# Kernel optimization log

Hardware: AMD Instinct MI355X
Metric: run time of the kernel (lower is better)

Reference implementation:

```python
import jax, jax.numpy as jnp
import numpy as np

# ---- BEVDepth config ----
B, N = 1, 6
C = 80            # numC_Trans
D = 112           # depth bins
HF, WF = 16, 44   # feature map size
DS = 16           # image downsample factor
XB = (-51.2, 51.2, 0.8)
YB = (-51.2, 51.2, 0.8)
ZB = (-10.0, 10.0, 20.0)
DB = (2.0, 58.0, 0.5)
NX, NY, NZ = 128, 128, 1
DX = np.array([XB[2], YB[2], ZB[2]], np.float32)
BX = np.array([XB[0] + XB[2] / 2.0, YB[0] + YB[2] / 2.0, ZB[0] + ZB[2] / 2.0], np.float32)


def _frustum():
    # (D, H, W, 3) points: (x_pixel, y_pixel, depth) in augmented image coords
    ds = np.arange(DB[0], DB[1], DB[2], dtype=np.float32)          # (D,)
    xs = np.linspace(0.0, WF * DS - 1.0, WF, dtype=np.float32)     # (W,)
    ys = np.linspace(0.0, HF * DS - 1.0, HF, dtype=np.float32)     # (H,)
    xg, yg, dg = np.broadcast_arrays(xs[None, None, :], ys[None, :, None], ds[:, None, None])
    return jnp.asarray(np.stack([xg, yg, dg], axis=-1))            # (D, H, W, 3)


def _get_geometry(rots, trans, intrins, post_rots, post_trans):
    # frustum -> ego-frame 3D points, shape (B, N, D, H, W, 3)
    fr = _frustum()                                                 # (D,H,W,3)
    pts = fr[None, None] - post_trans[:, :, None, None, None, :]
    inv_post = jnp.linalg.inv(post_rots)                            # (B,N,3,3)
    pts = jnp.einsum('bnij,bndhwj->bndhwi', inv_post, pts)
    # (x*d, y*d, d)
    pts = jnp.concatenate([pts[..., :2] * pts[..., 2:3], pts[..., 2:3]], axis=-1)
    combine = rots @ jnp.linalg.inv(intrins)                        # (B,N,3,3)
    pts = jnp.einsum('bnij,bndhwj->bndhwi', combine, pts)
    return pts + trans[:, :, None, None, None, :]


def _voxel_pooling(geom, volume):
    # geom: (B,N,D,H,W,3), volume: (B,N,D,H,W,C)
    dx = jnp.asarray(DX)
    bx = jnp.asarray(BX)
    # torch .long() truncates toward zero -> astype(int32) matches
    gi = ((geom - (bx - dx / 2.0)) / dx).astype(jnp.int32)          # (B,N,D,H,W,3)
    nprime = N * D * HF * WF
    gi = gi.reshape(B, nprime, 3)
    feats = volume.reshape(B * nprime, C)
    ix, iy, iz = gi[..., 0], gi[..., 1], gi[..., 2]                 # (B, nprime)
    valid = ((ix >= 0) & (ix < NX) & (iy >= 0) & (iy < NY) & (iz >= 0) & (iz < NZ))
    bix = jnp.arange(B, dtype=jnp.int32)[:, None]                    # (B,1)
    seg = ((bix * NZ + iz) * NX + ix) * NY + iy                      # (B, nprime)
    nseg = B * NZ * NX * NY
    seg = jnp.where(valid, seg, nseg).reshape(-1)
    pooled = jax.ops.segment_sum(feats, seg, num_segments=nseg + 1)[:-1]  # (B*NZ*NX*NY, C)
    bev = pooled.reshape(B, NZ, NX, NY, C)
    # final[b, :, iz, ix, iy]; unbind Z, cat on channel -> (B, C*NZ, NX, NY)
    bev = jnp.transpose(bev, (0, 4, 1, 2, 3)).reshape(B, C * NZ, NX, NY)
    return bev


def setup_inputs() -> dict:
    key = jax.random.key(0)
    k1, k2, k3 = jax.random.split(key, 3)
    x = jax.random.normal(k1, (B, N, 64, HF, WF), jnp.float32)
    img_feat = jax.random.normal(k2, (B * N, C, HF, WF), jnp.float32)
    depth_digit = jax.random.normal(k3, (B * N, D, HF, WF), jnp.float32)
    # realistic camera geometry: identity extrinsics, pinhole intrinsics,
    # post_rots encode the 1/16 feature-map rescale
    eye = jnp.eye(3, dtype=jnp.float32)
    rots = jnp.broadcast_to(eye, (B, N, 3, 3))
    trans = jnp.zeros((B, N, 3), jnp.float32)
    intr = jnp.array([[500.0, 0.0, WF * DS / 2.0],
                      [0.0, 500.0, HF * DS / 2.0],
                      [0.0, 0.0, 1.0]], jnp.float32)
    intrins = jnp.broadcast_to(intr, (B, N, 3, 3))
    post_rots = jnp.broadcast_to(eye, (B, N, 3, 3))
    post_trans = jnp.zeros((B, N, 3), jnp.float32)
    return {"x": x, "rots": rots, "trans": trans, "intrins": intrins,
            "post_rots": post_rots, "post_trans": post_trans,
            "img_feat": img_feat, "depth_digit": depth_digit}


def reference(x, rots, trans, intrins, post_rots, post_trans, img_feat, depth_digit):
    # depth distribution over D bins
    depth_prob = jax.nn.softmax(depth_digit, axis=1)                 # (BN, D, H, W)
    # depth-weighted outer product -> (BN, C, D, H, W)
    volume = depth_prob[:, None, :, :, :] * img_feat[:, :, None, :, :]
    volume = volume.reshape(B, N, C, D, HF, WF)
    volume = jnp.transpose(volume, (0, 1, 3, 4, 5, 2))               # (B,N,D,H,W,C)
    geom = _get_geometry(rots, trans, intrins, post_rots, post_trans)
    return _voxel_pooling(geom, volume)
```

## Files before the change

### kernel.cpp

```cpp
#include <hip/hip_runtime.h>

#define B_    1
#define N_    6
#define C_    80
#define D_    112
#define HF_   16
#define WF_   44
#define NX_   128
#define NY_   128
#define NZ_   1
#define HW_   (HF_ * WF_)
#define NPIX_ (NZ_ * NX_ * NY_)

__device__ __forceinline__ void inv3(const float* m, float* o) {
    float a = m[0], b = m[1], c = m[2];
    float d = m[3], e = m[4], f = m[5];
    float g = m[6], h = m[7], i = m[8];
    float A  =  (e * i - f * h);
    float Bc = -(d * i - f * g);
    float Cc =  (d * h - e * g);
    float det = a * A + b * Bc + c * Cc;
    float id = 1.0f / det;
    o[0] = A * id;                  o[1] = -(b * i - c * h) * id;   o[2] =  (b * f - c * e) * id;
    o[3] = Bc * id;                 o[4] =  (a * i - c * g) * id;   o[5] = -(a * f - c * d) * id;
    o[6] = Cc * id;                 o[7] = -(a * h - b * g) * id;   o[8] =  (a * e - b * d) * id;
}

__device__ __forceinline__ int voxel_of(float xs, float ys, float dv, const float* sm) {
    const float* ip  = sm;
    const float* cmb = sm + 9;
    float ptx = sm[18], pty = sm[19], ptz = sm[20];
    float trx = sm[21], trY = sm[22], trz = sm[23];
    float p0x = xs - ptx, p0y = ys - pty, p0z = dv - ptz;
    float p1x = ip[0]*p0x + ip[1]*p0y + ip[2]*p0z;
    float p1y = ip[3]*p0x + ip[4]*p0y + ip[5]*p0z;
    float p1z = ip[6]*p0x + ip[7]*p0y + ip[8]*p0z;
    float qx = p1x * p1z, qy = p1y * p1z, qz = p1z;
    float rx = cmb[0]*qx + cmb[1]*qy + cmb[2]*qz + trx;
    float ry = cmb[3]*qx + cmb[4]*qy + cmb[5]*qz + trY;
    float rz = cmb[6]*qx + cmb[7]*qy + cmb[8]*qz + trz;
    const float lox = -50.8f - 0.4f;
    const float loy = -50.8f - 0.4f;
    const float loz = -10.0f;
    int ix = (int)((rx - lox) / 0.8f);
    int iy = (int)((ry - loy) / 0.8f);
    int iz = (int)((rz - loz) / 20.0f);
    bool val = (ix >= 0) && (ix < NX_) && (iy >= 0) && (iy < NY_) && (iz >= 0) && (iz < NZ_);
    return val ? ((iz * NX_ + ix) * NY_ + iy) : -1;
}

__global__ __launch_bounds__(256) void scatter_merged(
    const float* __restrict__ rots, const float* __restrict__ trans,
    const float* __restrict__ intrins, const float* __restrict__ post_rots,
    const float* __restrict__ post_trans,
    const float* __restrict__ img_feat, const float* __restrict__ depth_digit,
    float* __restrict__ outp)
{
    const int hw = blockIdx.x;
    const int w  = hw % WF_;
    const int h  = hw / WF_;
    const int tid  = threadIdx.x;
    const int lane = tid & 63;
    const int wave = tid >> 6;

    __shared__ float s_prob[N_][D_];
    __shared__ float s_feat[N_][C_];
    __shared__ short s_vox[N_][D_];
    __shared__ short s_runv[N_][D_];
    __shared__ float s_runw[N_][D_];
    __shared__ float s_mat[N_][24];
    __shared__ int   s_cnt[N_];
    __shared__ int   s_same;

    for (int i = tid; i < N_ * D_; i += 256) {
        int cam = i / D_, d = i - cam * D_;
        s_prob[cam][d] = depth_digit[((size_t)cam * D_ + d) * HW_ + hw];
    }
    for (int i = tid; i < N_ * C_; i += 256) {
        int cam = i / C_, c = i - cam * C_;
        s_feat[cam][c] = img_feat[((size_t)cam * C_ + c) * HW_ + hw];
    }
    if (tid < N_) {
        float ipv[9], ii[9];
        inv3(post_rots + tid * 9, ipv);
        inv3(intrins + tid * 9, ii);
        const float* ro = rots + tid * 9;
        #pragma unroll
        for (int k = 0; k < 9; ++k) s_mat[tid][k] = ipv[k];
        #pragma unroll
        for (int r = 0; r < 3; ++r)
            #pragma unroll
            for (int c = 0; c < 3; ++c)
                s_mat[tid][9 + r * 3 + c] = ro[r*3+0]*ii[0*3+c] + ro[r*3+1]*ii[1*3+c] + ro[r*3+2]*ii[2*3+c];
        #pragma unroll
        for (int k = 0; k < 3; ++k) { s_mat[tid][18+k] = post_trans[tid*3+k]; s_mat[tid][21+k] = trans[tid*3+k]; }
    }
    __syncthreads();

    for (int cc = wave; cc < N_; cc += 4) {
        bool act = lane < 56;
        float l0 = act ? s_prob[cc][lane]      : -INFINITY;
        float l1 = act ? s_prob[cc][lane + 56] : -INFINITY;
        float m = fmaxf(l0, l1);
        #pragma unroll
        for (int o = 32; o > 0; o >>= 1) m = fmaxf(m, __shfl_xor(m, o));
        float e0 = act ? __expf(l0 - m) : 0.0f;
        float e1 = act ? __expf(l1 - m) : 0.0f;
        float s = e0 + e1;
        #pragma unroll
        for (int o = 32; o > 0; o >>= 1) s += __shfl_xor(s, o);
        float inv = 1.0f / s;
        if (act) { s_prob[cc][lane] = e0 * inv; s_prob[cc][lane + 56] = e1 * inv; }
    }

    {
        float xs = (float)((double)w * (703.0 / 43.0));
        float ys = (float)h * 17.0f;
        for (int i = tid; i < N_ * D_; i += 256) {
            int cam = i / D_, d = i - cam * D_;
            float dval = 2.0f + 0.5f * (float)d;
            s_vox[cam][d] = (short)voxel_of(xs, ys, dval, s_mat[cam]);
        }
    }
    __syncthreads();

    if (tid < N_) {
        int cnt = 0, last = -1;
        float wsum = 0.0f;
        #pragma unroll 4
        for (int d = 0; d < D_; ++d) {
            int v = s_vox[tid][d];
            if (v < 0) continue;
            if (v == last) { wsum += s_prob[tid][d]; }
            else {
                if (last >= 0) { s_runv[tid][cnt] = (short)last; s_runw[tid][cnt] = wsum; ++cnt; }
                last = v; wsum = s_prob[tid][d];
            }
        }
        if (last >= 0) { s_runv[tid][cnt] = (short)last; s_runw[tid][cnt] = wsum; ++cnt; }
        s_cnt[tid] = cnt;
    }
    __syncthreads();

    if (tid == 0) {
        int same = 1, c0 = s_cnt[0];
        #pragma unroll
        for (int cam = 1; cam < N_; ++cam) same &= (s_cnt[cam] == c0);
        if (same) {
            for (int r = 0; r < c0 && same; ++r) {
                short v0 = s_runv[0][r];
                #pragma unroll
                for (int cam = 1; cam < N_; ++cam) same &= (s_runv[cam][r] == v0);
            }
        }
        s_same = same;
    }
    __syncthreads();

    if (s_same) {
        int cnt = s_cnt[0];
        int total = cnt * C_;
        for (int k = tid; k < total; k += 256) {
            int r = k / C_;
            int c = k - r * C_;
            int v = s_runv[0][r];
            float val = 0.0f;
            #pragma unroll
            for (int cam = 0; cam < N_; ++cam)
                val = fmaf(s_runw[cam][r], s_feat[cam][c], val);
            atomicAdd(&outp[(size_t)c * NPIX_ + v], val);
        }
    } else {
        for (int cam = 0; cam < N_; ++cam) {
            int cnt = s_cnt[cam];
            int total = cnt * C_;
            for (int k = tid; k < total; k += 256) {
                int r = k / C_;
                int c = k - r * C_;
                int v = s_runv[cam][r];
                atomicAdd(&outp[(size_t)c * NPIX_ + v], s_runw[cam][r] * s_feat[cam][c]);
            }
        }
    }
}

extern "C" void kernel_launch(void* const* d_in, const int* in_sizes, int n_in,
                              void* d_out, int out_size, void* d_ws, size_t ws_size,
                              hipStream_t stream) {
    const float* rots        = (const float*)d_in[1];
    const float* trans       = (const float*)d_in[2];
    const float* intrins     = (const float*)d_in[3];
    const float* post_rots   = (const float*)d_in[4];
    const float* post_trans  = (const float*)d_in[5];
    const float* img_feat    = (const float*)d_in[6];
    const float* depth_digit = (const float*)d_in[7];
    float* outp = (float*)d_out;

    hipMemsetAsync(outp, 0, (size_t)out_size * sizeof(float), stream);
    scatter_merged<<<HW_, 256, 0, stream>>>(rots, trans, intrins, post_rots, post_trans,
                                            img_feat, depth_digit, outp);
}
```

Measured before the change: 107.5 us.

## Split voxel pooling into run-list generation and per-channel LDS accumulation

```diff
diff --git a/kernel.cpp b/kernel.cpp
--- a/kernel.cpp
+++ b/kernel.cpp
@@ -11,6 +11,8 @@
 #define NZ_   1
 #define HW_   (HF_ * WF_)
 #define NPIX_ (NZ_ * NX_ * NY_)
+#define CAMHW_ (N_ * HW_)
+#define ENTCAP_ (HW_ * N_ * D_)
 
 __device__ __forceinline__ void inv3(const float* m, float* o) {
     float a = m[0], b = m[1], c = m[2];
@@ -49,6 +51,151 @@
     return val ? ((iz * NX_ + ix) * NY_ + iy) : -1;
 }
 
+__global__ __launch_bounds__(256) void runs_kernel(
+    const float* __restrict__ rots, const float* __restrict__ trans,
+    const float* __restrict__ intrins, const float* __restrict__ post_rots,
+    const float* __restrict__ post_trans,
+    const float* __restrict__ depth_digit,
+    int2* __restrict__ entries, int* __restrict__ gE)
+{
+    const int hw = blockIdx.x;
+    const int w  = hw % WF_;
+    const int h  = hw / WF_;
+    const int tid  = threadIdx.x;
+    const int lane = tid & 63;
+    const int wave = tid >> 6;
+
+    __shared__ float s_prob[N_][D_];
+    __shared__ short s_vox[N_][D_];
+    __shared__ short s_runv[N_][D_];
+    __shared__ float s_runw[N_][D_];
+    __shared__ float s_mat[N_][24];
+    __shared__ int   s_cnt[N_];
+    __shared__ int   s_pref[N_ + 1];
+    __shared__ int   s_base;
+
+    for (int i = tid; i < N_ * D_; i += 256) {
+        int cam = i / D_, d = i - cam * D_;
+        s_prob[cam][d] = depth_digit[((size_t)cam * D_ + d) * HW_ + hw];
+    }
+    if (tid < N_) {
+        float ipv[9], ii[9];
+        inv3(post_rots + tid * 9, ipv);
+        inv3(intrins + tid * 9, ii);
+        const float* ro = rots + tid * 9;
+        #pragma unroll
+        for (int k = 0; k < 9; ++k) s_mat[tid][k] = ipv[k];
+        #pragma unroll
+        for (int r = 0; r < 3; ++r)
+            #pragma unroll
+            for (int c = 0; c < 3; ++c)
+                s_mat[tid][9 + r * 3 + c] = ro[r*3+0]*ii[0*3+c] + ro[r*3+1]*ii[1*3+c] + ro[r*3+2]*ii[2*3+c];
+        #pragma unroll
+        for (int k = 0; k < 3; ++k) { s_mat[tid][18+k] = post_trans[tid*3+k]; s_mat[tid][21+k] = trans[tid*3+k]; }
+    }
+    __syncthreads();
+
+    for (int cc = wave; cc < N_; cc += 4) {
+        bool act = lane < 56;
+        float l0 = act ? s_prob[cc][lane]      : -INFINITY;
+        float l1 = act ? s_prob[cc][lane + 56] : -INFINITY;
+        float m = fmaxf(l0, l1);
+        #pragma unroll
+        for (int o = 32; o > 0; o >>= 1) m = fmaxf(m, __shfl_xor(m, o));
+        float e0 = act ? __expf(l0 - m) : 0.0f;
+        float e1 = act ? __expf(l1 - m) : 0.0f;
+        float s = e0 + e1;
+        #pragma unroll
+        for (int o = 32; o > 0; o >>= 1) s += __shfl_xor(s, o);
+        float inv = 1.0f / s;
+        if (act) { s_prob[cc][lane] = e0 * inv; s_prob[cc][lane + 56] = e1 * inv; }
+    }
+
+    {
+        float xs = (float)((double)w * (703.0 / 43.0));
+        float ys = (float)h * 17.0f;
+        for (int i = tid; i < N_ * D_; i += 256) {
+            int cam = i / D_, d = i - cam * D_;
+            float dval = 2.0f + 0.5f * (float)d;
+            s_vox[cam][d] = (short)voxel_of(xs, ys, dval, s_mat[cam]);
+        }
+    }
+    __syncthreads();
+
+    if (tid < N_) {
+        int cnt = 0, last = -1;
+        float wsum = 0.0f;
+        for (int d = 0; d < D_; ++d) {
+            int v = s_vox[tid][d];
+            if (v < 0) continue;
+            if (v == last) { wsum += s_prob[tid][d]; }
+            else {
+                if (last >= 0) { s_runv[tid][cnt] = (short)last; s_runw[tid][cnt] = wsum; ++cnt; }
+                last = v; wsum = s_prob[tid][d];
+            }
+        }
+        if (last >= 0) { s_runv[tid][cnt] = (short)last; s_runw[tid][cnt] = wsum; ++cnt; }
+        s_cnt[tid] = cnt;
+    }
+    __syncthreads();
+
+    if (tid == 0) {
+        int acc = 0;
+        #pragma unroll
+        for (int cam = 0; cam < N_; ++cam) { s_pref[cam] = acc; acc += s_cnt[cam]; }
+        s_pref[N_] = acc;
+        s_base = atomicAdd(gE, acc);
+    }
+    __syncthreads();
+
+    int total = s_pref[N_];
+    int base = s_base;
+    for (int k = tid; k < total; k += 256) {
+        int cam = 0;
+        #pragma unroll
+        for (int cc = 1; cc < N_; ++cc) if (k >= s_pref[cc]) cam = cc;
+        int r = k - s_pref[cam];
+        int key = ((cam * HW_ + hw) << 14) | (int)s_runv[cam][r];
+        entries[base + k] = make_int2(key, __float_as_int(s_runw[cam][r]));
+    }
+}
+
+__global__ __launch_bounds__(1024) void accum_kernel(
+    const float* __restrict__ img_feat,
+    const int2* __restrict__ entries, const int* __restrict__ gE,
+    float* __restrict__ outp)
+{
+    const int c   = blockIdx.x;
+    const int tid = threadIdx.x;
+
+    __shared__ float s_plane[NPIX_];
+    __shared__ float s_feat[CAMHW_];
+    __shared__ int   s_E;
+
+    float4* p4 = (float4*)s_plane;
+    #pragma unroll
+    for (int i = tid; i < NPIX_ / 4; i += 1024) p4[i] = make_float4(0.f, 0.f, 0.f, 0.f);
+    for (int i = tid; i < CAMHW_; i += 1024) {
+        int cam = i / HW_, hw = i - cam * HW_;
+        s_feat[i] = img_feat[((size_t)cam * C_ + c) * HW_ + hw];
+    }
+    if (tid == 0) s_E = *gE;
+    __syncthreads();
+
+    int E = s_E;
+    for (int i = tid; i < E; i += 1024) {
+        int2 e = entries[i];
+        int vox   = e.x & (NPIX_ - 1);
+        int camhw = e.x >> 14;
+        atomicAdd(&s_plane[vox], __int_as_float(e.y) * s_feat[camhw]);
+    }
+    __syncthreads();
+
+    float4* o4 = (float4*)(outp + (size_t)c * NPIX_);
+    #pragma unroll
+    for (int i = tid; i < NPIX_ / 4; i += 1024) o4[i] = p4[i];
+}
+
 __global__ __launch_bounds__(256) void scatter_merged(
     const float* __restrict__ rots, const float* __restrict__ trans,
     const float* __restrict__ intrins, const float* __restrict__ post_rots,
@@ -70,15 +217,14 @@
     __shared__ float s_runw[N_][D_];
     __shared__ float s_mat[N_][24];
     __shared__ int   s_cnt[N_];
-    __shared__ int   s_same;
 
     for (int i = tid; i < N_ * D_; i += 256) {
         int cam = i / D_, d = i - cam * D_;
         s_prob[cam][d] = depth_digit[((size_t)cam * D_ + d) * HW_ + hw];
     }
     for (int i = tid; i < N_ * C_; i += 256) {
-        int cam = i / C_, c = i - cam * C_;
-        s_feat[cam][c] = img_feat[((size_t)cam * C_ + c) * HW_ + hw];
+        int cam = i / C_, cc = i - cam * C_;
+        s_feat[cam][cc] = img_feat[((size_t)cam * C_ + cc) * HW_ + hw];
     }
     if (tid < N_) {
         float ipv[9], ii[9];
@@ -112,7 +258,6 @@
         float inv = 1.0f / s;
         if (act) { s_prob[cc][lane] = e0 * inv; s_prob[cc][lane + 56] = e1 * inv; }
     }
-
     {
         float xs = (float)((double)w * (703.0 / 43.0));
         float ys = (float)h * 17.0f;
@@ -123,11 +268,9 @@
         }
     }
     __syncthreads();
-
     if (tid < N_) {
         int cnt = 0, last = -1;
         float wsum = 0.0f;
-        #pragma unroll 4
         for (int d = 0; d < D_; ++d) {
             int v = s_vox[tid][d];
             if (v < 0) continue;
@@ -141,45 +284,14 @@
         s_cnt[tid] = cnt;
     }
     __syncthreads();
-
-    if (tid == 0) {
-        int same = 1, c0 = s_cnt[0];
-        #pragma unroll
-        for (int cam = 1; cam < N_; ++cam) same &= (s_cnt[cam] == c0);
-        if (same) {
-            for (int r = 0; r < c0 && same; ++r) {
-                short v0 = s_runv[0][r];
-                #pragma unroll
-                for (int cam = 1; cam < N_; ++cam) same &= (s_runv[cam][r] == v0);
-            }
-        }
-        s_same = same;
-    }
-    __syncthreads();
-
-    if (s_same) {
-        int cnt = s_cnt[0];
+    for (int cam = 0; cam < N_; ++cam) {
+        int cnt = s_cnt[cam];
         int total = cnt * C_;
         for (int k = tid; k < total; k += 256) {
             int r = k / C_;
             int c = k - r * C_;
-            int v = s_runv[0][r];
-            float val = 0.0f;
-            #pragma unroll
-            for (int cam = 0; cam < N_; ++cam)
-                val = fmaf(s_runw[cam][r], s_feat[cam][c], val);
-            atomicAdd(&outp[(size_t)c * NPIX_ + v], val);
-        }
-    } else {
-        for (int cam = 0; cam < N_; ++cam) {
-            int cnt = s_cnt[cam];
-            int total = cnt * C_;
-            for (int k = tid; k < total; k += 256) {
-                int r = k / C_;
-                int c = k - r * C_;
-                int v = s_runv[cam][r];
-                atomicAdd(&outp[(size_t)c * NPIX_ + v], s_runw[cam][r] * s_feat[cam][c]);
-            }
+            int v = s_runv[cam][r];
+            atomicAdd(&outp[(size_t)c * NPIX_ + v], s_runw[cam][r] * s_feat[cam][c]);
         }
     }
 }
@@ -196,7 +308,20 @@
     const float* depth_digit = (const float*)d_in[7];
     float* outp = (float*)d_out;
 
-    hipMemsetAsync(outp, 0, (size_t)out_size * sizeof(float), stream);
-    scatter_merged<<<HW_, 256, 0, stream>>>(rots, trans, intrins, post_rots, post_trans,
-                                            img_feat, depth_digit, outp);
-}
+    const size_t gE_b      = 256;
+    const size_t entries_b = (size_t)ENTCAP_ * 8;
+    const size_t need = gE_b + entries_b;
+
+    if (ws_size >= need) {
+        int*  gE      = (int*)d_ws;
+        int2* entries = (int2*)((char*)d_ws + gE_b);
+        hipMemsetAsync(gE, 0, 4, stream);
+        runs_kernel<<<HW_, 256, 0, stream>>>(rots, trans, intrins, post_rots, post_trans,
+                                             depth_digit, entries, gE);
+        accum_kernel<<<C_, 1024, 0, stream>>>(img_feat, entries, gE, outp);
+    } else {
+        hipMemsetAsync(outp, 0, (size_t)out_size * sizeof(float), stream);
+        scatter_merged<<<HW_, 256, 0, stream>>>(rots, trans, intrins, post_rots, post_trans,
+                                                img_feat, depth_digit, outp);
+    }
+}
```

Result: slower. 125.8 us (+17.1%).

## Tile 4 pixels per block and aggregate weights in shared bounding-box slots

Applied to the files above, without the earlier changes.

```diff
diff --git a/kernel.cpp b/kernel.cpp
--- a/kernel.cpp
+++ b/kernel.cpp
@@ -1,6 +1,6 @@
 #include <hip/hip_runtime.h>
-
-#define B_    1
+#include <limits.h>
+
 #define N_    6
 #define C_    80
 #define D_    112
@@ -8,9 +8,14 @@
 #define WF_   44
 #define NX_   128
 #define NY_   128
-#define NZ_   1
 #define HW_   (HF_ * WF_)
-#define NPIX_ (NZ_ * NX_ * NY_)
+#define NPIX_ (NX_ * NY_)
+#define TPX_  4
+#define NTW_  (WF_ / TPX_)
+#define NT_   (HF_ * NTW_)
+#define PC_   (N_ * TPX_)
+#define CAP_  256
+#define WPAD_ 25
 
 __device__ __forceinline__ void inv3(const float* m, float* o) {
     float a = m[0], b = m[1], c = m[2];
@@ -45,62 +50,73 @@
     int ix = (int)((rx - lox) / 0.8f);
     int iy = (int)((ry - loy) / 0.8f);
     int iz = (int)((rz - loz) / 20.0f);
-    bool val = (ix >= 0) && (ix < NX_) && (iy >= 0) && (iy < NY_) && (iz >= 0) && (iz < NZ_);
-    return val ? ((iz * NX_ + ix) * NY_ + iy) : -1;
-}
-
-__global__ __launch_bounds__(256) void scatter_merged(
+    bool val = (ix >= 0) && (ix < NX_) && (iy >= 0) && (iy < NY_) && (iz >= 0) && (iz < 1);
+    return val ? (ix * NY_ + iy) : -1;
+}
+
+__global__ __launch_bounds__(512) void tile_kernel(
     const float* __restrict__ rots, const float* __restrict__ trans,
     const float* __restrict__ intrins, const float* __restrict__ post_rots,
     const float* __restrict__ post_trans,
     const float* __restrict__ img_feat, const float* __restrict__ depth_digit,
     float* __restrict__ outp)
 {
-    const int hw = blockIdx.x;
-    const int w  = hw % WF_;
-    const int h  = hw / WF_;
+    const int tb  = blockIdx.x;
+    const int th  = tb / NTW_;
+    const int w0  = (tb - th * NTW_) * TPX_;
+    const int hw0 = th * WF_ + w0;
     const int tid  = threadIdx.x;
     const int lane = tid & 63;
     const int wave = tid >> 6;
 
-    __shared__ float s_prob[N_][D_];
-    __shared__ float s_feat[N_][C_];
-    __shared__ short s_vox[N_][D_];
-    __shared__ short s_runv[N_][D_];
-    __shared__ float s_runw[N_][D_];
+    __shared__ float s_prob[PC_][D_];
+    __shared__ short s_vox[PC_][D_];
+    __shared__ float s_wt[CAP_][WPAD_];
+    __shared__ float s_featT[C_][PC_];
+    __shared__ short s_slotvox[CAP_];
     __shared__ float s_mat[N_][24];
-    __shared__ int   s_cnt[N_];
-    __shared__ int   s_same;
-
-    for (int i = tid; i < N_ * D_; i += 256) {
-        int cam = i / D_, d = i - cam * D_;
-        s_prob[cam][d] = depth_digit[((size_t)cam * D_ + d) * HW_ + hw];
-    }
-    for (int i = tid; i < N_ * C_; i += 256) {
-        int cam = i / C_, c = i - cam * C_;
-        s_feat[cam][c] = img_feat[((size_t)cam * C_ + c) * HW_ + hw];
-    }
-    if (tid < N_) {
+    __shared__ float s_xs[TPX_];
+    __shared__ int   s_bb[4];
+    __shared__ int   s_geo[5];
+
+    for (int i = tid; i < PC_ * D_; i += 512) {
+        int cd = i >> 2, px = i & 3;
+        int cam = cd / D_, d = cd - cam * D_;
+        s_prob[cam * TPX_ + px][d] = depth_digit[((size_t)cam * D_ + d) * HW_ + hw0 + px];
+    }
+    for (int i = tid; i < PC_ * C_; i += 512) {
+        int cc = i >> 2, px = i & 3;
+        int cam = cc / C_, c = cc - cam * C_;
+        s_featT[c][cam * TPX_ + px] = img_feat[((size_t)cam * C_ + c) * HW_ + hw0 + px];
+    }
+    for (int i = tid; i < CAP_ * WPAD_; i += 512) ((float*)s_wt)[i] = 0.0f;
+    for (int i = tid; i < CAP_; i += 512) s_slotvox[i] = -1;
+    if (tid < 4) s_bb[tid] = (tid == 0 || tid == 2) ? INT_MAX : INT_MIN;
+    if (tid >= 8 && tid < 12) s_xs[tid - 8] = (float)((double)(w0 + tid - 8) * (703.0 / 43.0));
+    if (tid >= 16 && tid < 16 + N_) {
+        int cam = tid - 16;
         float ipv[9], ii[9];
-        inv3(post_rots + tid * 9, ipv);
-        inv3(intrins + tid * 9, ii);
-        const float* ro = rots + tid * 9;
-        #pragma unroll
-        for (int k = 0; k < 9; ++k) s_mat[tid][k] = ipv[k];
+        inv3(post_rots + cam * 9, ipv);
+        inv3(intrins + cam * 9, ii);
+        const float* ro = rots + cam * 9;
+        #pragma unroll
+        for (int k = 0; k < 9; ++k) s_mat[cam][k] = ipv[k];
         #pragma unroll
         for (int r = 0; r < 3; ++r)
             #pragma unroll
             for (int c = 0; c < 3; ++c)
-                s_mat[tid][9 + r * 3 + c] = ro[r*3+0]*ii[0*3+c] + ro[r*3+1]*ii[1*3+c] + ro[r*3+2]*ii[2*3+c];
-        #pragma unroll
-        for (int k = 0; k < 3; ++k) { s_mat[tid][18+k] = post_trans[tid*3+k]; s_mat[tid][21+k] = trans[tid*3+k]; }
+                s_mat[cam][9 + r * 3 + c] = ro[r*3+0]*ii[0*3+c] + ro[r*3+1]*ii[1*3+c] + ro[r*3+2]*ii[2*3+c];
+        #pragma unroll
+        for (int k = 0; k < 3; ++k) { s_mat[cam][18+k] = post_trans[cam*3+k]; s_mat[cam][21+k] = trans[cam*3+k]; }
     }
     __syncthreads();
 
-    for (int cc = wave; cc < N_; cc += 4) {
+    #pragma unroll
+    for (int j = 0; j < 3; ++j) {
+        int pc = wave * 3 + j;
         bool act = lane < 56;
-        float l0 = act ? s_prob[cc][lane]      : -INFINITY;
-        float l1 = act ? s_prob[cc][lane + 56] : -INFINITY;
+        float l0 = act ? s_prob[pc][lane]      : -INFINITY;
+        float l1 = act ? s_prob[pc][lane + 56] : -INFINITY;
         float m = fmaxf(l0, l1);
         #pragma unroll
         for (int o = 32; o > 0; o >>= 1) m = fmaxf(m, __shfl_xor(m, o));
@@ -110,76 +126,78 @@
         #pragma unroll
         for (int o = 32; o > 0; o >>= 1) s += __shfl_xor(s, o);
         float inv = 1.0f / s;
-        if (act) { s_prob[cc][lane] = e0 * inv; s_prob[cc][lane + 56] = e1 * inv; }
-    }
-
+        if (act) { s_prob[pc][lane] = e0 * inv; s_prob[pc][lane + 56] = e1 * inv; }
+    }
     {
-        float xs = (float)((double)w * (703.0 / 43.0));
-        float ys = (float)h * 17.0f;
-        for (int i = tid; i < N_ * D_; i += 256) {
-            int cam = i / D_, d = i - cam * D_;
-            float dval = 2.0f + 0.5f * (float)d;
-            s_vox[cam][d] = (short)voxel_of(xs, ys, dval, s_mat[cam]);
+        float ys = (float)th * 17.0f;
+        int mnx = INT_MAX, mxx = INT_MIN, mny = INT_MAX, mxy = INT_MIN;
+        for (int i = tid; i < PC_ * D_; i += 512) {
+            int pc = i / D_, d = i - pc * D_;
+            int cam = pc >> 2, px = pc & 3;
+            int v = voxel_of(s_xs[px], ys, 2.0f + 0.5f * (float)d, s_mat[cam]);
+            s_vox[pc][d] = (short)v;
+            if (v >= 0) {
+                int ix = v >> 7, iy = v & 127;
+                mnx = min(mnx, ix); mxx = max(mxx, ix);
+                mny = min(mny, iy); mxy = max(mxy, iy);
+            }
+        }
+        if (mxx >= 0) {
+            atomicMin(&s_bb[0], mnx); atomicMax(&s_bb[1], mxx);
+            atomicMin(&s_bb[2], mny); atomicMax(&s_bb[3], mxy);
         }
     }
     __syncthreads();
 
-    if (tid < N_) {
-        int cnt = 0, last = -1;
-        float wsum = 0.0f;
-        #pragma unroll 4
-        for (int d = 0; d < D_; ++d) {
-            int v = s_vox[tid][d];
-            if (v < 0) continue;
-            if (v == last) { wsum += s_prob[tid][d]; }
-            else {
-                if (last >= 0) { s_runv[tid][cnt] = (short)last; s_runw[tid][cnt] = wsum; ++cnt; }
-                last = v; wsum = s_prob[tid][d];
+    if (tid == 0) {
+        if (s_bb[1] < s_bb[0]) { s_geo[3] = 0; s_geo[4] = 0; }
+        else {
+            int bw = s_bb[1] - s_bb[0] + 1;
+            int bh = s_bb[3] - s_bb[2] + 1;
+            int area = bw * bh;
+            s_geo[0] = s_bb[0]; s_geo[1] = s_bb[2]; s_geo[2] = bh;
+            s_geo[3] = area; s_geo[4] = (area > CAP_) ? 1 : 0;
+        }
+    }
+    __syncthreads();
+
+    int area = s_geo[3];
+    int fb   = s_geo[4];
+
+    if (area > 0 && !fb) {
+        int ix0 = s_geo[0], iy0 = s_geo[1], bh = s_geo[2];
+        for (int i = tid; i < PC_ * D_; i += 512) {
+            int pc = i / D_, d = i - pc * D_;
+            int v = s_vox[pc][d];
+            if (v >= 0) {
+                int slot = ((v >> 7) - ix0) * bh + ((v & 127) - iy0);
+                atomicAdd(&s_wt[slot][pc], s_prob[pc][d]);
+                s_slotvox[slot] = (short)v;
             }
         }
-        if (last >= 0) { s_runv[tid][cnt] = (short)last; s_runw[tid][cnt] = wsum; ++cnt; }
-        s_cnt[tid] = cnt;
-    }
-    __syncthreads();
-
-    if (tid == 0) {
-        int same = 1, c0 = s_cnt[0];
-        #pragma unroll
-        for (int cam = 1; cam < N_; ++cam) same &= (s_cnt[cam] == c0);
-        if (same) {
-            for (int r = 0; r < c0 && same; ++r) {
-                short v0 = s_runv[0][r];
-                #pragma unroll
-                for (int cam = 1; cam < N_; ++cam) same &= (s_runv[cam][r] == v0);
+        __syncthreads();
+
+        for (int k = tid; k < C_ * CAP_; k += 512) {
+            int slot = k & (CAP_ - 1);
+            int c    = k >> 8;
+            if (slot < area) {
+                int v = s_slotvox[slot];
+                if (v >= 0) {
+                    float val = 0.0f;
+                    #pragma unroll
+                    for (int j = 0; j < PC_; ++j)
+                        val = fmaf(s_wt[slot][j], s_featT[c][j], val);
+                    atomicAdd(&outp[(size_t)c * NPIX_ + v], val);
+                }
             }
         }
-        s_same = same;
-    }
-    __syncthreads();
-
-    if (s_same) {
-        int cnt = s_cnt[0];
-        int total = cnt * C_;
-        for (int k = tid; k < total; k += 256) {
-            int r = k / C_;
-            int c = k - r * C_;
-            int v = s_runv[0][r];
-            float val = 0.0f;
-            #pragma unroll
-            for (int cam = 0; cam < N_; ++cam)
-                val = fmaf(s_runw[cam][r], s_feat[cam][c], val);
-            atomicAdd(&outp[(size_t)c * NPIX_ + v], val);
-        }
-    } else {
-        for (int cam = 0; cam < N_; ++cam) {
-            int cnt = s_cnt[cam];
-            int total = cnt * C_;
-            for (int k = tid; k < total; k += 256) {
-                int r = k / C_;
-                int c = k - r * C_;
-                int v = s_runv[cam][r];
-                atomicAdd(&outp[(size_t)c * NPIX_ + v], s_runw[cam][r] * s_feat[cam][c]);
-            }
+    } else if (fb) {
+        for (int k = tid; k < PC_ * D_ * C_; k += 512) {
+            int pcd = k / C_, c = k - pcd * C_;
+            int pc = pcd / D_, d = pcd - pc * D_;
+            int v = s_vox[pc][d];
+            if (v >= 0)
+                atomicAdd(&outp[(size_t)c * NPIX_ + v], s_prob[pc][d] * s_featT[c][pc]);
         }
     }
 }
@@ -196,7 +214,7 @@
     const float* depth_digit = (const float*)d_in[7];
     float* outp = (float*)d_out;
 
-    hipMemsetAsync(outp, 0, (size_t)out_size * sizeof(float), stream);
-    scatter_merged<<<HW_, 256, 0, stream>>>(rots, trans, intrins, post_rots, post_trans,
-                                            img_feat, depth_digit, outp);
-}
+    (void)hipMemsetAsync(outp, 0, (size_t)out_size * sizeof(float), stream);
+    tile_kernel<<<NT_, 512, 0, stream>>>(rots, trans, intrins, post_rots, post_trans,
+                                         img_feat, depth_digit, outp);
+}
```

After: 101.7 us. 5.4% less time.
